# Kernel tuning notes

Hardware: AMD Instinct MI355X
Metric: run time of the kernel (lower is better)

Reference implementation:

```python
import jax, jax.numpy as jnp
import numpy as np

D_MODEL = 2048
N_HEADS = 16
HEAD_DIM = D_MODEL // N_HEADS
B, T = 2, 2048


def setup_inputs() -> dict:
    key = jax.random.key(0)
    ks = jax.random.split(key, 5)
    s = 1.0 / np.sqrt(D_MODEL)
    x = jax.random.normal(ks[0], (B, T, D_MODEL), dtype=jnp.float32)
    Wq = jax.random.uniform(ks[1], (D_MODEL, D_MODEL), jnp.float32, -s, s)
    Wk = jax.random.uniform(ks[2], (D_MODEL, D_MODEL), jnp.float32, -s, s)
    Wv = jax.random.uniform(ks[3], (D_MODEL, D_MODEL), jnp.float32, -s, s)
    Wo = jax.random.uniform(ks[4], (D_MODEL, D_MODEL), jnp.float32, -s, s)
    return {"x": x, "Wq": Wq, "Wk": Wk, "Wv": Wv, "Wo": Wo}


def _alibi_bias(n_heads: int, seq_len: int) -> jnp.ndarray:
    # slopes_h = 0.5 ** (h * 8 / n_heads), h = 1..n_heads
    exponents = jnp.arange(1, n_heads + 1, dtype=jnp.float32)
    slopes = 0.5 ** (exponents * 8.0 / n_heads)  # (H,)
    pos = jnp.arange(seq_len, dtype=jnp.float32)
    rel = pos[None, :] - pos[:, None]  # (T,T), rel[i,j] = j - i
    bias = slopes[:, None, None] * rel[None]  # (H,T,T)
    causal = pos[None, :] <= pos[:, None]  # j <= i
    return jnp.where(causal[None], bias, -jnp.inf)


def reference(x, Wq, Wk, Wv, Wo):
    Bsz, Tlen, _ = x.shape
    H, D = N_HEADS, HEAD_DIM
    # projections (nn.Linear: x @ W.T); split heads -> (B,H,T,D)
    def split_heads(t):
        return t.reshape(Bsz, Tlen, H, D).transpose(0, 2, 1, 3)
    q = split_heads(x @ Wq.T)
    k = split_heads(x @ Wk.T)
    v = split_heads(x @ Wv.T)
    scale = jnp.sqrt(jnp.float32(D))
    scores = jnp.einsum('bhqd,bhkd->bhqk', q, k) / scale  # (B,H,T,T)
    scores = scores + _alibi_bias(H, Tlen)[None]
    attn = jax.nn.softmax(scores, axis=-1)
    out = jnp.einsum('bhqk,bhkd->bhqd', attn, v)
    out = out.transpose(0, 2, 1, 3).reshape(Bsz, Tlen, H * D)
    return out @ Wo.T
```

## Files before the change

kernel.cpp:

```cpp
#include <hip/hip_runtime.h>
#include <stdint.h>

#define D_MODEL 2048
#define N_HEADS 16
#define HEAD_D  128
#define BATCH   2
#define SEQ     2048
#define MTOT    (BATCH*SEQ)

typedef __bf16 bf16x8 __attribute__((ext_vector_type(8)));
typedef float  f32x4  __attribute__((ext_vector_type(4)));
typedef unsigned short u16x8 __attribute__((ext_vector_type(8)));
typedef unsigned short u16x4 __attribute__((ext_vector_type(4)));

#define MFMA16(a,b,c) __builtin_amdgcn_mfma_f32_16x16x32_bf16(a, b, c, 0, 0, 0)

__device__ __forceinline__ unsigned short f2bf(float f) {
  unsigned u = __builtin_bit_cast(unsigned, f);
  u += 0x7fffu + ((u >> 16) & 1u);
  return (unsigned short)(u >> 16);
}

__device__ __forceinline__ bf16x8 ld_frag(const unsigned short* p) {
  u16x8 raw = *(const u16x8*)p;
  return __builtin_bit_cast(bf16x8, raw);
}

__device__ __forceinline__ void gload16(const void* g, void* lds) {
  __builtin_amdgcn_global_load_lds(
      (const __attribute__((address_space(1))) unsigned int*)g,
      (__attribute__((address_space(3))) unsigned int*)lds, 16, 0, 0);
}

__global__ __launch_bounds__(256) void f32_to_bf16_k(const float* __restrict__ in,
                                                     unsigned short* __restrict__ out,
                                                     int n8) {
  int i = blockIdx.x * 256 + threadIdx.x;
  if (i >= n8) return;
  const float4* p = (const float4*)in + (size_t)i * 2;
  float4 a = p[0], b = p[1];
  u16x8 o;
  o[0] = f2bf(a.x); o[1] = f2bf(a.y); o[2] = f2bf(a.z); o[3] = f2bf(a.w);
  o[4] = f2bf(b.x); o[5] = f2bf(b.y); o[6] = f2bf(b.z); o[7] = f2bf(b.w);
  *((u16x8*)out + i) = o;
}

__global__ __launch_bounds__(256) void f32_to_bf16_w4(const float* __restrict__ w0,
                                                      const float* __restrict__ w1,
                                                      const float* __restrict__ w2,
                                                      const float* __restrict__ w3,
                                                      unsigned short* __restrict__ out) {
  const int i = blockIdx.x * 256 + threadIdx.x;
  const int which = i >> 19;
  const int r = i & ((1 << 19) - 1);
  const float* s = (which == 0) ? w0 : (which == 1) ? w1 : (which == 2) ? w2 : w3;
  const float4* p = (const float4*)s + (size_t)r * 2;
  float4 a = p[0], b = p[1];
  u16x8 o;
  o[0] = f2bf(a.x); o[1] = f2bf(a.y); o[2] = f2bf(a.z); o[3] = f2bf(a.w);
  o[4] = f2bf(b.x); o[5] = f2bf(b.y); o[6] = f2bf(b.z); o[7] = f2bf(b.w);
  *((u16x8*)out + i) = o;
}

__global__ __launch_bounds__(256) void gemm_bt_f32(const unsigned short* __restrict__ A,
                                                   const unsigned short* __restrict__ B,
                                                   float* __restrict__ C,
                                                   int M, int N, int K) {
  __shared__ __align__(16) unsigned short As[128 * 32];
  __shared__ __align__(16) unsigned short Bs[128 * 32];
  const int tid  = threadIdx.x;
  const int lane = tid & 63;
  const int w    = tid >> 6;
  const int wr   = w >> 1, wc = w & 1;

  const int gx = gridDim.x;
  int bx = blockIdx.x, by = blockIdx.y;
  const int nwg = gx * gridDim.y;
  if ((nwg & 7) == 0) {
    const int lid = by * gx + bx;
    const int cpx = nwg >> 3;
    const int swz = (lid & 7) * cpx + (lid >> 3);
    bx = swz % gx; by = swz / gx;
  }
  const int brow = by * 128;
  const int bcol = bx * 128;

  const int e0 = (w * 2) * 512 + lane * 8;
  const int e1 = (w * 2 + 1) * 512 + lane * 8;
  const int r0 = e0 >> 5, cc0 = e0 & 31;
  const int r1 = e1 >> 5, cc1 = e1 & 31;
  const unsigned short* Ap0 = A + (size_t)(brow + r0) * K + cc0;
  const unsigned short* Ap1 = A + (size_t)(brow + r1) * K + cc1;
  const unsigned short* Bp0 = B + (size_t)(bcol + r0) * K + cc0;
  const unsigned short* Bp1 = B + (size_t)(bcol + r1) * K + cc1;
  unsigned short* As0 = &As[(w * 2) * 512];
  unsigned short* As1 = &As[(w * 2 + 1) * 512];
  unsigned short* Bs0 = &Bs[(w * 2) * 512];
  unsigned short* Bs1 = &Bs[(w * 2 + 1) * 512];

  f32x4 acc[4][4] = {};
  const int la = lane & 15;
  const int lb = (lane >> 4) * 8;

  for (int kt = 0; kt < K; kt += 32) {
    gload16(Ap0 + kt, As0);
    gload16(Ap1 + kt, As1);
    gload16(Bp0 + kt, Bs0);
    gload16(Bp1 + kt, Bs1);
    __syncthreads();
    bf16x8 af[4], bfr[4];
#pragma unroll
    for (int m = 0; m < 4; ++m)
      af[m] = ld_frag(&As[(wr * 64 + m * 16 + la) * 32 + lb]);
#pragma unroll
    for (int n = 0; n < 4; ++n)
      bfr[n] = ld_frag(&Bs[(wc * 64 + n * 16 + la) * 32 + lb]);
#pragma unroll
    for (int m = 0; m < 4; ++m)
#pragma unroll
      for (int n = 0; n < 4; ++n)
        acc[m][n] = MFMA16(af[m], bfr[n], acc[m][n]);
    __syncthreads();
  }

  const int rowb = (lane >> 4) * 4;
#pragma unroll
  for (int m = 0; m < 4; ++m)
#pragma unroll
    for (int n = 0; n < 4; ++n) {
      const int gcol = bcol + wc * 64 + n * 16 + la;
      const int grow0 = brow + wr * 64 + m * 16 + rowb;
#pragma unroll
      for (int j = 0; j < 4; ++j)
        C[(size_t)(grow0 + j) * N + gcol] = acc[m][n][j];
    }
}


#define SQ_STAGE_HALF(T2, HF)                                                     \
  do {                                                                            \
    const int kt2_ = (T2) * 64;                                                   \
    _Pragma("unroll")                                                             \
    for (int s_ = 0; s_ < 2; ++s_) {                                              \
      const int idx_ = s_ * 512 + tid;                                            \
      const int sub_ = idx_ >> 6;                                                 \
      const int rin_ = (idx_ >> 2) & 15;                                          \
      const int cby_ = (idx_ & 3) * 16;                                           \
      const int r_   = ((HF) & 1) * 128 + (sub_ >> 1) * 16 + rin_;                \
      const int ce_  = (sub_ & 1) * 32 + ((cby_ ^ ((rin_ & 8) << 2)) >> 1);       \
      const unsigned short* gp_ = ((HF) < 2)                                      \
          ? (Ag + (size_t)(brow + r_) * 2048 + kt2_ + ce_)                        \
          : (Bg + (size_t)(bcol + r_) * 2048 + kt2_ + ce_);                       \
      gload16(gp_, SB + ((((T2) & 1) * 65536 + ((HF) >> 1) * 32768 +              \
                          ((HF) & 1) * 16384 + (s_ * 512 + w * 64) * 16) >> 1));  \
    }                                                                             \
  } while (0)

#define SQ_STAGE_ALL(T2)                                                          \
  do { SQ_STAGE_HALF(T2, 0); SQ_STAGE_HALF(T2, 1);                                \
       SQ_STAGE_HALF(T2, 2); SQ_STAGE_HALF(T2, 3); } while (0)

#define SQ_PHASE2(CUR, KK)                                                        \
  do {                                                                            \
    bf16x8 af_[8];                                                                \
    bf16x8 bf_[4];                                                                \
    const char* Ab_ = (const char*)SB + (CUR) * 65536 + wr * 16384;               \
    const char* Bb_ = (const char*)SB + (CUR) * 65536 + 32768 +                   \
                      (wcn >> 1) * 16384 + (wcn & 1) * 8192;                      \
    _Pragma("unroll")                                                             \
    for (int m_ = 0; m_ < 8; ++m_)                                                \
      af_[m_] = ld_frag((const unsigned short*)(Ab_ + m_ * 2048 +                 \
                                                (KK) * 1024 + la * 64 + cxa));    \
    _Pragma("unroll")                                                             \
    for (int n_ = 0; n_ < 4; ++n_)                                                \
      bf_[n_] = ld_frag((const unsigned short*)(Bb_ + n_ * 2048 +                 \
                                                (KK) * 1024 + la * 64 + cxa));    \
    asm volatile("s_waitcnt lgkmcnt(0)" ::: "memory");                            \
    __builtin_amdgcn_sched_barrier(0);                                            \
    __builtin_amdgcn_s_setprio(1);                                                \
    _Pragma("unroll")                                                             \
    for (int m_ = 0; m_ < 8; ++m_)                                                \
      _Pragma("unroll")                                                           \
      for (int n_ = 0; n_ < 4; ++n_)                                              \
        acc[m_][n_] = MFMA16(af_[m_], bf_[n_], acc[m_][n_]);                      \
    __builtin_amdgcn_s_setprio(0);                                                \
  } while (0)

__global__ __launch_bounds__(512, 1)
__attribute__((amdgpu_waves_per_eu(1, 2)))
void gemm_qkv256(const unsigned short* __restrict__ Ag,
                 const unsigned short* __restrict__ Bg,
                 unsigned short* __restrict__ Qp,
                 unsigned short* __restrict__ Kp,
                 unsigned short* __restrict__ Vtp) {
  __shared__ __align__(16) unsigned short SB[65536];
  const int tid = threadIdx.x, lane = tid & 63, w = tid >> 6;
  const int wr = w >> 2, wcn = w & 3;
  const int la = lane & 15, hi = lane >> 4;
  const int cxa = (hi * 16) ^ ((lane & 8) << 2);

  const int gx = gridDim.x;
  const int nwg = gx * gridDim.y;
  const int lid = blockIdx.y * gx + blockIdx.x;
  const int cpx = nwg >> 3;
  const int sz = (lid & 7) * cpx + (lid >> 3);
  const int bx = sz % gx, by = sz / gx;
  const int brow = by * 256, bcol = bx * 256;

  f32x4 acc[8][4] = {};

  SQ_STAGE_ALL(0);

#pragma unroll 1
  for (int t = 0; t < 32; ++t) {
    const int cur = t & 1;
    if (t < 31) {
      SQ_STAGE_ALL(t + 1);
      asm volatile("s_waitcnt vmcnt(8)" ::: "memory");
    } else {
      asm volatile("s_waitcnt vmcnt(0)" ::: "memory");
    }
    __builtin_amdgcn_sched_barrier(0);
    __builtin_amdgcn_s_barrier();

    SQ_PHASE2(cur, 0);
    SQ_PHASE2(cur, 1);

    __builtin_amdgcn_s_barrier();
  }

#pragma unroll
  for (int mg = 0; mg < 8; ++mg) {
#pragma unroll
    for (int ng = 0; ng < 4; ++ng) {
      const int gcol = bcol + wcn * 64 + ng * 16 + la;
      const int grow0 = brow + wr * 128 + mg * 16 + hi * 4;
      const int which = gcol >> 11;
      const int c2 = gcol & 2047;
      const int hh = c2 >> 7, dd = c2 & 127;
      const int bb = grow0 >> 11, tt = grow0 & (SEQ - 1);
      if (which == 2) {
        u16x4 pk;
#pragma unroll
        for (int j = 0; j < 4; ++j) pk[j] = f2bf(acc[mg][ng][j]);
        *(u16x4*)&Vtp[(((size_t)bb * N_HEADS + hh) * HEAD_D + dd) * SEQ + tt] = pk;
      } else {
        unsigned short* dst = which ? Kp : Qp;
#pragma unroll
        for (int j = 0; j < 4; ++j)
          dst[(((size_t)bb * N_HEADS + hh) * SEQ + tt + j) * HEAD_D + dd] = f2bf(acc[mg][ng][j]);
      }
    }
  }
}

#define STAGE_KV(U, BSEL)                                                           \
  do {                                                                              \
    const int kv0_ = (((U) <= qtA) ? (U) : (U) - qtA - 1) * 64;                     \
    _Pragma("unroll")                                                               \
    for (int s = 0; s < 4; ++s) {                                                   \
      const int p_ = (w * 4 + s) * 1024 + lane * 16;                                \
      const int row_ = p_ >> 8, cb_ = p_ & 255;                                     \
      const int col_ = (cb_ ^ ((row_ & 7) << 4)) >> 1;                              \
      gload16(&K[kbase + (size_t)(kv0_ + row_) * HEAD_D + col_],                    \
              &Ks[BSEL][(w * 4 + s) * 512]);                                        \
    }                                                                               \
    _Pragma("unroll")                                                               \
    for (int s = 0; s < 4; ++s) {                                                   \
      const int p_ = (w * 4 + s) * 1024 + lane * 16;                                \
      const int d_ = p_ >> 7, cb_ = p_ & 127;                                       \
      const int col_ = (cb_ ^ ((d_ & 7) << 4)) >> 1;                                \
      gload16(&VT[vtbase + (size_t)d_ * SEQ + kv0_ + col_],                         \
              &Vs[BSEL][(w * 4 + s) * 512]);                                        \
    }                                                                               \
  } while (0)

#define LOAD_Q(Q0)                                                                  \
  do {                                                                              \
    const size_t qa_ = ((size_t)bh * SEQ + (Q0) + w * 16 + la) * HEAD_D + lq * 8;   \
    _Pragma("unroll")                                                               \
    for (int kk = 0; kk < 4; ++kk) qf[kk] = ld_frag(&Q[qa_ + kk * 32]);             \
  } while (0)

#define EPILOGUE(Q0)                                                                \
  do {                                                                              \
    _Pragma("unroll")                                                               \
    for (int j = 0; j < 4; ++j) {                                                   \
      const float inv_ = 1.0f / lrow[j];                                            \
      const int q_ = (Q0) + w * 16 + lq * 4 + j;                                    \
      const size_t ob_ = ((size_t)b * SEQ + q_) * D_MODEL + (size_t)h * HEAD_D;     \
      _Pragma("unroll")                                                             \
      for (int n = 0; n < 8; ++n) O[ob_ + n * 16 + la] = f2bf(acc[n][j] * inv_);    \
    }                                                                               \
  } while (0)

#define SOFTMAX_TILE(S, QG0, DIAG, KV0)                                            \
  do {                                                                             \
    float corr_[4];                                                                \
    float pe_[4][4];                                                               \
    _Pragma("unroll")                                                              \
    for (int j = 0; j < 4; ++j) {                                                  \
      const int qgj_ = (QG0) + j;                                                  \
      float mx_ = -1e30f;                                                          \
      _Pragma("unroll")                                                            \
      for (int c = 0; c < 4; ++c) {                                                \
        const int kvg_ = (KV0) + c * 16 + la;                                      \
        float sv_ = fmaf(S[c][j], scale, slope * (float)(kvg_ - qgj_));            \
        if ((DIAG) && (kvg_ > qgj_)) sv_ = -1e30f;                                 \
        pe_[c][j] = sv_;                                                           \
        mx_ = fmaxf(mx_, sv_);                                                     \
      }                                                                            \
      mx_ = fmaxf(mx_, __shfl_xor(mx_, 1));                                        \
      mx_ = fmaxf(mx_, __shfl_xor(mx_, 2));                                        \
      mx_ = fmaxf(mx_, __shfl_xor(mx_, 4));                                        \
      mx_ = fmaxf(mx_, __shfl_xor(mx_, 8));                                        \
      const float nm_ = fmaxf(mrow[j], mx_);                                       \
      const float cr_ = __expf(mrow[j] - nm_);                                     \
      corr_[j] = cr_;                                                              \
      float rs_ = 0.f;                                                             \
      _Pragma("unroll")                                                            \
      for (int c = 0; c < 4; ++c) {                                                \
        const float e_ = __expf(pe_[c][j] - nm_);                                  \
        pe_[c][j] = e_;                                                            \
        rs_ += e_;                                                                 \
      }                                                                            \
      rs_ += __shfl_xor(rs_, 1);                                                   \
      rs_ += __shfl_xor(rs_, 2);                                                   \
      rs_ += __shfl_xor(rs_, 4);                                                   \
      rs_ += __shfl_xor(rs_, 8);                                                   \
      lrow[j] = lrow[j] * cr_ + rs_;                                               \
      mrow[j] = nm_;                                                               \
    }                                                                              \
    _Pragma("unroll")                                                              \
    for (int n = 0; n < 8; ++n) {                                                  \
      _Pragma("unroll")                                                            \
      for (int j = 0; j < 4; ++j) acc[n][j] *= corr_[j];                           \
    }                                                                              \
    _Pragma("unroll")                                                              \
    for (int c = 0; c < 4; ++c) {                                                  \
      _Pragma("unroll")                                                            \
      for (int j = 0; j < 4; ++j) {                                                \
        const int row_ = lq * 4 + j;                                               \
        const int cb_ = (c * 16 + la) * 2;                                         \
        *(unsigned short*)((char*)Ps[w] + row_ * 128 + (cb_ ^ ((row_ & 7) << 4)))  \
            = f2bf(pe_[c][j]);                                                     \
      }                                                                            \
    }                                                                              \
  } while (0)

__global__ __launch_bounds__(256)
void attn_k(const unsigned short* __restrict__ Q,
            const unsigned short* __restrict__ K,
            const unsigned short* __restrict__ VT,
            unsigned short* __restrict__ O) {
  __shared__ __align__(16) unsigned short Ks[2][64 * HEAD_D];
  __shared__ __align__(16) unsigned short Vs[2][HEAD_D * 64];
  __shared__ __align__(16) unsigned short Ps[4][16 * 64];

  const int tid = threadIdx.x, lane = tid & 63, w = tid >> 6;
  const int lid = blockIdx.x;
  const int swz = (lid & 7) * 64 + (lid >> 3);
  const int qp = swz & 15;
  const int h  = (swz >> 4) & 15;
  const int b  = swz >> 8;
  const int bh = b * N_HEADS + h;
  const int qtA = qp, qtB = 31 - qp;
  const int q0A = qtA * 64, q0B = qtB * 64;

  const float slope = exp2f(-0.5f * (float)(h + 1));
  const float scale = 0.08838834764831845f;
  const int la = lane & 15;
  const int lq = lane >> 4;

  const size_t kbase  = (size_t)bh * SEQ * HEAD_D;
  const size_t vtbase = (size_t)bh * HEAD_D * SEQ;

  bf16x8 qf[4];
  f32x4 acc[8] = {};
  float mrow[4] = {-1e30f, -1e30f, -1e30f, -1e30f};
  float lrow[4] = {0.f, 0.f, 0.f, 0.f};
  int q0cur = q0A;

  LOAD_Q(q0A);
  STAGE_KV(0, 0);

  for (int u = 0; u < 33; ++u) {
    if (u < 32) {
      STAGE_KV(u + 1, (u + 1) & 1);
      asm volatile("s_waitcnt vmcnt(8)" ::: "memory");
    } else {
      asm volatile("s_waitcnt vmcnt(0)" ::: "memory");
    }
    __builtin_amdgcn_sched_barrier(0);
    __builtin_amdgcn_s_barrier();

    if (u == qtA + 1) {
      EPILOGUE(q0A);
      LOAD_Q(q0B);
      q0cur = q0B;
#pragma unroll
      for (int n = 0; n < 8; ++n)
#pragma unroll
        for (int j = 0; j < 4; ++j) acc[n][j] = 0.f;
#pragma unroll
      for (int j = 0; j < 4; ++j) { mrow[j] = -1e30f; lrow[j] = 0.f; }
    }

    const int cur = u & 1;
    const int kv0 = ((u <= qtA) ? u : u - qtA - 1) * 64;
    const bool diag = (u == qtA) || (u == 32);

    f32x4 s4[4] = {{0.f,0.f,0.f,0.f},{0.f,0.f,0.f,0.f},{0.f,0.f,0.f,0.f},{0.f,0.f,0.f,0.f}};
    __builtin_amdgcn_s_setprio(1);
#pragma unroll
    for (int c = 0; c < 4; ++c) {
      const int row = c * 16 + la;
#pragma unroll
      for (int kk = 0; kk < 4; ++kk) {
        const int cb = kk * 64 + lq * 16;
        bf16x8 kf = ld_frag((const unsigned short*)((const char*)Ks[cur] + row * 256 + (cb ^ ((row & 7) << 4))));
        s4[c] = MFMA16(qf[kk], kf, s4[c]);
      }
    }
    __builtin_amdgcn_s_setprio(0);

    SOFTMAX_TILE(s4, q0cur + w * 16 + lq * 4, diag, kv0);

    asm volatile("s_waitcnt lgkmcnt(0)" ::: "memory");
    __builtin_amdgcn_sched_barrier(0);

    __builtin_amdgcn_s_setprio(1);
#pragma unroll
    for (int kk = 0; kk < 2; ++kk) {
      const int pcb = kk * 64 + lq * 16;
      const int paddr = la * 128 + (pcb ^ ((la & 7) << 4));
      bf16x8 pf = ld_frag((const unsigned short*)((const char*)Ps[w] + paddr));
#pragma unroll
      for (int n = 0; n < 8; ++n) {
        const int d = n * 16 + la;
        bf16x8 vf = ld_frag((const unsigned short*)((const char*)Vs[cur] + d * 128 + (pcb ^ ((d & 7) << 4))));
        acc[n] = MFMA16(pf, vf, acc[n]);
      }
    }
    __builtin_amdgcn_s_setprio(0);

    __builtin_amdgcn_s_barrier();
  }

  EPILOGUE(q0B);
}

extern "C" void kernel_launch(void* const* d_in, const int* in_sizes, int n_in,
                              void* d_out, int out_size, void* d_ws, size_t ws_size,
                              hipStream_t stream) {
  (void)in_sizes; (void)n_in; (void)out_size; (void)ws_size;
  const float* x  = (const float*)d_in[0];
  const float* Wq = (const float*)d_in[1];
  const float* Wk = (const float*)d_in[2];
  const float* Wv = (const float*)d_in[3];
  const float* Wo = (const float*)d_in[4];

  char* ws = (char*)d_ws;
  unsigned short* xb = (unsigned short*)(ws + 0);
  unsigned short* wq = (unsigned short*)(ws + 16777216);
  unsigned short* wo = (unsigned short*)(ws + 41943040);
  unsigned short* q  = (unsigned short*)(ws + 50331648);
  unsigned short* k  = (unsigned short*)(ws + 67108864);
  unsigned short* vt = (unsigned short*)(ws + 83886080);
  unsigned short* o  = (unsigned short*)(ws + 0);

  f32_to_bf16_k<<<4096, 256, 0, stream>>>(x, xb, (MTOT * D_MODEL) / 8);
  f32_to_bf16_w4<<<8192, 256, 0, stream>>>(Wq, Wk, Wv, Wo, wq);

  gemm_qkv256<<<dim3(3 * D_MODEL / 256, MTOT / 256), 512, 0, stream>>>(xb, wq, q, k, vt);

  attn_k<<<512, 256, 0, stream>>>(q, k, vt, o);

  dim3 g2(D_MODEL / 128, MTOT / 128);
  gemm_bt_f32<<<g2, 256, 0, stream>>>(o, wo, (float*)d_out, MTOT, D_MODEL, D_MODEL);
}
```

Before: 297.6 us.

## Retile QKV GEMM to 256x128 tiles with 256 threads and K-step 32

Changes the fused QKV projection GEMM from a 256x256 tile with 512 threads and K-step 64 to a 256x128 tile with 256 threads and K-step 32. Shared memory drops from 128KB to 48KB, so more workgroups can fit per CU. The grid doubles in the column dimension and the main loop runs 64 iterations. Each workgroup now reuses each loaded A tile across half as many columns, and there are twice as many barriers per K. An unused SQ_STAGE macro is left in the file.

```diff
diff --git a/kernel.cpp b/kernel.cpp
--- a/kernel.cpp
+++ b/kernel.cpp
@@ -137,65 +137,46 @@
 }
 
 
-#define SQ_STAGE_HALF(T2, HF)                                                     \
+#define SQ_STAGE(TT, BSEL)                                                        \
   do {                                                                            \
-    const int kt2_ = (T2) * 64;                                                   \
+    const int kt_ = (TT) * 32;                                                    \
     _Pragma("unroll")                                                             \
-    for (int s_ = 0; s_ < 2; ++s_) {                                              \
-      const int idx_ = s_ * 512 + tid;                                            \
+    for (int s_ = 0; s_ < 4; ++s_) {                          \
+      const int idx_ = s_ * 256 + tid;                                            \
       const int sub_ = idx_ >> 6;                                                 \
-      const int rin_ = (idx_ >> 2) & 15;                                          \
-      const int cby_ = (idx_ & 3) * 16;                                           \
-      const int r_   = ((HF) & 1) * 128 + (sub_ >> 1) * 16 + rin_;                \
-      const int ce_  = (sub_ & 1) * 32 + ((cby_ ^ ((rin_ & 8) << 2)) >> 1);       \
-      const unsigned short* gp_ = ((HF) < 2)                                      \
-          ? (Ag + (size_t)(brow + r_) * 2048 + kt2_ + ce_)                        \
-          : (Bg + (size_t)(bcol + r_) * 2048 + kt2_ + ce_);                       \
-      gload16(gp_, SB + ((((T2) & 1) * 65536 + ((HF) >> 1) * 32768 +              \
-                          ((HF) & 1) * 16384 + (s_ * 512 + w * 64) * 16) >> 1));  \
+      const int g_   = idx_ & 63;                                                 \
+      const int rin_ = g_ >> 2;                                                   \
+      const int cby_ = (g_ & 3) * 16;                                             \
+      const int r_   = sub_ * 16 + rin_;                                          \
+      const int ce_  = (cby_ ^ ((rin_ & 8) << 2)) >> 1;                           \
+      gload16(Ag + (size_t)(brow + r_) * 2048 + kt_ + ce_,                        \
+              SB + (((BSEL) * 24576 + sub_ * 1024 + (tid >> 6) * 1024 +           \
+                     0 * 0) >> 1) + 0);                                           \
+    }                                                                             \
+    _Pragma("unroll")                                                             \
+    for (int s_ = 0; s_ < 2; ++s_) {                           \
+      const int idx_ = s_ * 256 + tid;                                            \
+      const int sub_ = idx_ >> 6;                                                 \
+      const int g_   = idx_ & 63;                                                 \
+      const int rin_ = g_ >> 2;                                                   \
+      const int cby_ = (g_ & 3) * 16;                                             \
+      const int r_   = sub_ * 16 + rin_;                                          \
+      const int ce_  = (cby_ ^ ((rin_ & 8) << 2)) >> 1;                           \
+      gload16(Bg + (size_t)(bcol + r_) * 2048 + kt_ + ce_,                        \
+              SB + (((BSEL) * 24576 + 16384 + sub_ * 1024) >> 1));                \
     }                                                                             \
   } while (0)
 
-#define SQ_STAGE_ALL(T2)                                                          \
-  do { SQ_STAGE_HALF(T2, 0); SQ_STAGE_HALF(T2, 1);                                \
-       SQ_STAGE_HALF(T2, 2); SQ_STAGE_HALF(T2, 3); } while (0)
-
-#define SQ_PHASE2(CUR, KK)                                                        \
-  do {                                                                            \
-    bf16x8 af_[8];                                                                \
-    bf16x8 bf_[4];                                                                \
-    const char* Ab_ = (const char*)SB + (CUR) * 65536 + wr * 16384;               \
-    const char* Bb_ = (const char*)SB + (CUR) * 65536 + 32768 +                   \
-                      (wcn >> 1) * 16384 + (wcn & 1) * 8192;                      \
-    _Pragma("unroll")                                                             \
-    for (int m_ = 0; m_ < 8; ++m_)                                                \
-      af_[m_] = ld_frag((const unsigned short*)(Ab_ + m_ * 2048 +                 \
-                                                (KK) * 1024 + la * 64 + cxa));    \
-    _Pragma("unroll")                                                             \
-    for (int n_ = 0; n_ < 4; ++n_)                                                \
-      bf_[n_] = ld_frag((const unsigned short*)(Bb_ + n_ * 2048 +                 \
-                                                (KK) * 1024 + la * 64 + cxa));    \
-    asm volatile("s_waitcnt lgkmcnt(0)" ::: "memory");                            \
-    __builtin_amdgcn_sched_barrier(0);                                            \
-    __builtin_amdgcn_s_setprio(1);                                                \
-    _Pragma("unroll")                                                             \
-    for (int m_ = 0; m_ < 8; ++m_)                                                \
-      _Pragma("unroll")                                                           \
-      for (int n_ = 0; n_ < 4; ++n_)                                              \
-        acc[m_][n_] = MFMA16(af_[m_], bf_[n_], acc[m_][n_]);                      \
-    __builtin_amdgcn_s_setprio(0);                                                \
-  } while (0)
-
-__global__ __launch_bounds__(512, 1)
-__attribute__((amdgpu_waves_per_eu(1, 2)))
+__global__ __launch_bounds__(256, 1)
+__attribute__((amdgpu_waves_per_eu(2, 2)))
 void gemm_qkv256(const unsigned short* __restrict__ Ag,
                  const unsigned short* __restrict__ Bg,
                  unsigned short* __restrict__ Qp,
                  unsigned short* __restrict__ Kp,
                  unsigned short* __restrict__ Vtp) {
-  __shared__ __align__(16) unsigned short SB[65536];
+  __shared__ __align__(16) unsigned short SB[24576];
   const int tid = threadIdx.x, lane = tid & 63, w = tid >> 6;
-  const int wr = w >> 2, wcn = w & 3;
+  const int wr = w >> 1, wcn = w & 1;
   const int la = lane & 15, hi = lane >> 4;
   const int cxa = (hi * 16) ^ ((lane & 8) << 2);
 
@@ -205,26 +186,74 @@
   const int cpx = nwg >> 3;
   const int sz = (lid & 7) * cpx + (lid >> 3);
   const int bx = sz % gx, by = sz / gx;
-  const int brow = by * 256, bcol = bx * 256;
+  const int brow = by * 256, bcol = bx * 128;
 
   f32x4 acc[8][4] = {};
 
-  SQ_STAGE_ALL(0);
+
+#define SQ_STAGE_V6(TT, BSEL)                                                     \
+  do {                                                                            \
+    const int kt_ = (TT) * 32;                                                    \
+    _Pragma("unroll")                                                             \
+    for (int s_ = 0; s_ < 4; ++s_) {                                              \
+      const int idx_ = s_ * 256 + tid;                                            \
+      const int sub_ = idx_ >> 6;                                                 \
+      const int g_   = idx_ & 63;                                                 \
+      const int rin_ = g_ >> 2;                                                   \
+      const int cby_ = (g_ & 3) * 16;                                             \
+      const int r_   = sub_ * 16 + rin_;                                          \
+      const int ce_  = (cby_ ^ ((rin_ & 8) << 2)) >> 1;                           \
+      gload16(Ag + (size_t)(brow + r_) * 2048 + kt_ + ce_,                        \
+              SB + (((BSEL) * 24576 + sub_ * 1024) >> 1));                        \
+    }                                                                             \
+    _Pragma("unroll")                                                             \
+    for (int s_ = 0; s_ < 2; ++s_) {                                              \
+      const int idx_ = s_ * 256 + tid;                                            \
+      const int sub_ = idx_ >> 6;                                                 \
+      const int g_   = idx_ & 63;                                                 \
+      const int rin_ = g_ >> 2;                                                   \
+      const int cby_ = (g_ & 3) * 16;                                             \
+      const int r_   = sub_ * 16 + rin_;                                          \
+      const int ce_  = (cby_ ^ ((rin_ & 8) << 2)) >> 1;                           \
+      gload16(Bg + (size_t)(bcol + r_) * 2048 + kt_ + ce_,                        \
+              SB + (((BSEL) * 24576 + 16384 + sub_ * 1024) >> 1));                \
+    }                                                                             \
+  } while (0)
+
+  SQ_STAGE_V6(0, 0);
 
 #pragma unroll 1
-  for (int t = 0; t < 32; ++t) {
+  for (int t = 0; t < 64; ++t) {
     const int cur = t & 1;
-    if (t < 31) {
-      SQ_STAGE_ALL(t + 1);
-      asm volatile("s_waitcnt vmcnt(8)" ::: "memory");
+    if (t < 63) {
+      SQ_STAGE_V6(t + 1, cur ^ 1);
+      asm volatile("s_waitcnt vmcnt(6)" ::: "memory");
     } else {
       asm volatile("s_waitcnt vmcnt(0)" ::: "memory");
     }
     __builtin_amdgcn_sched_barrier(0);
     __builtin_amdgcn_s_barrier();
 
-    SQ_PHASE2(cur, 0);
-    SQ_PHASE2(cur, 1);
+    {
+      const char* Ab_ = (const char*)SB + cur * 24576 + wr * 8192;
+      const char* Bb_ = (const char*)SB + cur * 24576 + 16384 + wcn * 4096;
+      bf16x8 afr_[8], bfr_[4];
+#pragma unroll
+      for (int m_ = 0; m_ < 8; ++m_)
+        afr_[m_] = ld_frag((const unsigned short*)(Ab_ + m_ * 1024 + la * 64 + cxa));
+#pragma unroll
+      for (int n_ = 0; n_ < 4; ++n_)
+        bfr_[n_] = ld_frag((const unsigned short*)(Bb_ + n_ * 1024 + la * 64 + cxa));
+      asm volatile("s_waitcnt lgkmcnt(0)" ::: "memory");
+      __builtin_amdgcn_sched_barrier(0);
+      __builtin_amdgcn_s_setprio(1);
+#pragma unroll
+      for (int m_ = 0; m_ < 8; ++m_)
+#pragma unroll
+        for (int n_ = 0; n_ < 4; ++n_)
+          acc[m_][n_] = MFMA16(afr_[m_], bfr_[n_], acc[m_][n_]);
+      __builtin_amdgcn_s_setprio(0);
+    }
 
     __builtin_amdgcn_s_barrier();
   }
@@ -472,7 +501,7 @@
   f32_to_bf16_k<<<4096, 256, 0, stream>>>(x, xb, (MTOT * D_MODEL) / 8);
   f32_to_bf16_w4<<<8192, 256, 0, stream>>>(Wq, Wk, Wv, Wo, wq);
 
-  gemm_qkv256<<<dim3(3 * D_MODEL / 256, MTOT / 256), 512, 0, stream>>>(xb, wq, q, k, vt);
+  gemm_qkv256<<<dim3(3 * D_MODEL / 128, MTOT / 256), 256, 0, stream>>>(xb, wq, q, k, vt);
 
   attn_k<<<512, 256, 0, stream>>>(q, k, vt, o);
 
```

Result: slower. 308.3 us (+3.6%).
